# Optimization experiments

Measured on AMD Instinct MI355X. Metric: run time of the kernel, lower is better.

The kernel has to match this reference:

```python
import jax, jax.numpy as jnp
import numpy as np

DIM = 256          # dim_m == dim_d (required by hist @ W1)
HIST = 200         # history_num
B = 2048
U_TOT = 100000
V_TOT = 100000
EPS = 1e-12


def _max_norm_lookup(table, idx):
    # torch nn.Embedding(max_norm=1): rows are renormalized to L2 norm <= 1 at lookup.
    g = table[idx]
    n = jnp.linalg.norm(g, axis=-1, keepdims=True)
    return g * jnp.minimum(1.0, 1.0 / jnp.maximum(n, EPS))


def _l2norm(x):
    # F.normalize(x, 2, -1)
    return x / jnp.maximum(jnp.linalg.norm(x, axis=-1, keepdims=True), EPS)


def setup_inputs() -> dict:
    key = jax.random.key(0)
    ks = jax.random.split(key, 12)
    xav = float(np.sqrt(6.0 / (DIM + DIM)))
    xav_pb = float(np.sqrt(6.0 / (HIST + DIM)))
    return {
        "batch_u": jax.random.randint(ks[0], (B,), 0, U_TOT),
        "batch_v": jax.random.randint(ks[1], (B,), 0, V_TOT),
        "batch_history": jax.random.randint(ks[2], (B, HIST), 0, V_TOT),
        "batch_olc": jax.random.randint(ks[3], (B,), 0, 68),
        "batch_cluster_olc": jax.random.randint(ks[4], (B,), 0, 68),
        "user_emb": jax.random.normal(ks[5], (U_TOT, DIM), jnp.float32),
        "venue_emb": jax.random.normal(ks[6], (V_TOT, DIM), jnp.float32),
        "W1": jax.random.uniform(ks[7], (DIM, DIM), jnp.float32, -xav, xav),
        "W2": jax.random.uniform(ks[8], (DIM, DIM), jnp.float32, -xav, xav),
        "P": jax.random.normal(ks[9], (HIST, DIM), jnp.float32),
        "bias": jax.random.uniform(ks[10], (HIST, DIM), jnp.float32, -xav_pb, xav_pb),
        "a": jax.random.normal(ks[11], (1,), jnp.float32),
    }


def reference(batch_u, batch_v, batch_history, batch_olc, batch_cluster_olc,
              user_emb, venue_emb, W1, W2, P, bias, a):
    # batch_olc / batch_cluster_olc are read but unused in the original forward.
    u = _max_norm_lookup(user_emb, batch_u)            # [B, D]
    v = _max_norm_lookup(venue_emb, batch_v)           # [B, D]
    hist = _max_norm_lookup(venue_emb, batch_history)  # [B, H, D]

    # h = tanh(hist @ W1 + (P @ W2) + bias), broadcast over batch
    h = jnp.tanh(jnp.einsum('bhd,de->bhe', hist, W1) + (P @ W2)[None] + bias[None])
    alpha = jax.nn.softmax(h, axis=1)                  # softmax over history dim
    l = jnp.sum(alpha * hist, axis=1) + a              # [B, D], scalar a broadcast

    # TransE-style score with p_norm = 2
    s = _l2norm(u) + _l2norm(l) - _l2norm(v)
    return jnp.sqrt(jnp.sum(s * s, axis=-1))           # [B]
```

## Files before the change

kernel.cpp:

```cpp
#include <hip/hip_runtime.h>

#define DIM 256
#define HIST 200
#define MPAD 208
#define BATCH 2048
#define HSTRIDE 264
#define EPSF 1e-12f

typedef __bf16 bf16x8 __attribute__((ext_vector_type(8)));
typedef float f32x4 __attribute__((ext_vector_type(4)));

__device__ __forceinline__ unsigned short f2bf(float f) {
    union { float f; unsigned u; } v; v.f = f;
    unsigned r = (v.u + 0x7fffu + ((v.u >> 16) & 1u)) >> 16;
    return (unsigned short)r;
}
__device__ __forceinline__ float bf2f(unsigned short u) {
    union { unsigned u; float f; } v; v.u = ((unsigned)u) << 16;
    return v.f;
}

__global__ __launch_bounds__(256) void k_prep(
    const float* __restrict__ W1, const float* __restrict__ P,
    const float* __restrict__ W2, const float* __restrict__ bias,
    const float* __restrict__ venue,
    unsigned short* __restrict__ W1t2, float* __restrict__ Ct2,
    float* __restrict__ sInv, int nV) {
    const int bid = blockIdx.x, tid = threadIdx.x;
    if (bid < 16) {
#pragma unroll
        for (int it = 0; it < 16; ++it) {
            int idx = bid * 4096 + it * 256 + tid;
            int g = idx >> 11, rem = idx & 2047;
            int n = rem >> 3, j = rem & 7;
            W1t2[idx] = f2bf(W1[(g * 8 + j) * DIM + n]);
        }
    } else if (bid < 224) {
        const int h = bid - 16;
        __shared__ float Prow[DIM];
        const int e = tid;
        float acc = 0.f;
        if (h < HIST) {
            Prow[e] = P[h * DIM + e];
            __syncthreads();
            acc = bias[h * DIM + e];
#pragma unroll 8
            for (int d = 0; d < DIM; ++d) acc += Prow[d] * W2[d * DIM + e];
        }
        Ct2[((h >> 4) * 4 + ((h >> 2) & 3)) * 1024 + e * 4 + (h & 3)] = acc;
    } else {
        const int row = (bid - 224) * 4 + (tid >> 6);
        if (row >= nV) return;
        const int lane = tid & 63;
        const float4 g = *(const float4*)(venue + (size_t)row * DIM + lane * 4);
        float ss = g.x * g.x + g.y * g.y + g.z * g.z + g.w * g.w;
#pragma unroll
        for (int off = 32; off > 0; off >>= 1) ss += __shfl_xor(ss, off);
        if (lane == 0) sInv[row] = fminf(1.f, 1.f / fmaxf(sqrtf(ss), EPSF));
    }
}

__global__ __launch_bounds__(1024, 4) void k_main(
    const int* __restrict__ batch_u, const int* __restrict__ batch_v,
    const int* __restrict__ batch_history,
    const float* __restrict__ user_emb, const float* __restrict__ venue_emb,
    const float* __restrict__ Ct2, const unsigned short* __restrict__ W1t2,
    const float* __restrict__ sInv,
    const float* __restrict__ a_ptr, float* __restrict__ out) {

    __shared__ unsigned short histS[MPAD * HSTRIDE];
    __shared__ float scaleS[MPAD];
    __shared__ int idxS[MPAD];
    __shared__ float lArr[DIM];
    __shared__ float redS[4][4];
    __shared__ float invS[3];

    const int b = blockIdx.x;
    const int tid = threadIdx.x;
    const int wave = tid >> 6;
    const int lane = tid & 63;
    const int quad = lane >> 4;
    const int l16 = lane & 15;
    const int n = wave * 16 + l16;

    if (tid < MPAD) {
        int m = (tid < HIST) ? tid : 0;
        int ix = batch_history[b * HIST + m];
        idxS[tid] = ix;
        scaleS[tid] = sInv[ix];
    }
    __syncthreads();

    const int r0 = wave * 13;
    float4 buf[13];
#pragma unroll
    for (int j = 0; j < 13; ++j)
        buf[j] = *(const float4*)(venue_emb + (size_t)idxS[r0 + j] * DIM + lane * 4);
#pragma unroll
    for (int j = 0; j < 13; ++j) {
        float s = scaleS[r0 + j];
        ushort4 pk = { f2bf(buf[j].x * s), f2bf(buf[j].y * s),
                       f2bf(buf[j].z * s), f2bf(buf[j].w * s) };
        *(ushort4*)&histS[(r0 + j) * HSTRIDE + lane * 4] = pk;
    }

    f32x4 acc[13];
#pragma unroll
    for (int mt = 0; mt < 13; ++mt)
        acc[mt] = *(const f32x4*)(Ct2 + (mt * 4 + quad) * 1024 + n * 4);

    float ut = 0.f, vt = 0.f;
    if (tid < DIM) {
        ut = user_emb[(size_t)batch_u[b] * DIM + tid];
        vt = venue_emb[(size_t)batch_v[b] * DIM + tid];
    }
    __syncthreads();

#pragma unroll
    for (int k = 0; k < 8; ++k) {
        const bf16x8 Bf = *(const bf16x8*)(const void*)(W1t2 + (k * 4 + quad) * 2048 + n * 8);
#pragma unroll
        for (int mt = 0; mt < 13; ++mt) {
            const bf16x8 Af =
                *(const bf16x8*)(const void*)(&histS[(mt * 16 + l16) * HSTRIDE + k * 32 + quad * 8]);
            acc[mt] = __builtin_amdgcn_mfma_f32_16x16x32_bf16(Af, Bf, acc[mt], 0, 0, 0);
        }
    }

    const float a_val = a_ptr[0];
    float Ssum = 0.f, Lnum = 0.f;
#pragma unroll
    for (int mt = 0; mt < 13; ++mt)
#pragma unroll
        for (int r = 0; r < 4; ++r) {
            int m = mt * 16 + quad * 4 + r;
            if (m < HIST) {
                float x = acc[mt][r];
                float e2 = __expf(2.f * x);
                float th = 1.f - 2.f / (e2 + 1.f);
                float e = __expf(th);
                Ssum += e;
                Lnum += e * bf2f(histS[m * HSTRIDE + n]);
            }
        }
    Ssum += __shfl_xor(Ssum, 16); Ssum += __shfl_xor(Ssum, 32);
    Lnum += __shfl_xor(Lnum, 16); Lnum += __shfl_xor(Lnum, 32);
    if (quad == 0) lArr[n] = Lnum / Ssum + a_val;
    __syncthreads();

    const float lt = (tid < DIM) ? lArr[tid] : 0.f;
    float pu = ut * ut, pv = vt * vt, pl = lt * lt;
#pragma unroll
    for (int off = 32; off > 0; off >>= 1) {
        pu += __shfl_xor(pu, off);
        pv += __shfl_xor(pv, off);
        pl += __shfl_xor(pl, off);
    }
    if (lane == 0 && wave < 4) { redS[wave][0] = pu; redS[wave][1] = pv; redS[wave][2] = pl; }
    __syncthreads();
    if (tid == 0) {
        float su = 0.f, sv = 0.f, sl = 0.f;
        for (int w = 0; w < 4; ++w) { su += redS[w][0]; sv += redS[w][1]; sl += redS[w][2]; }
        invS[0] = 1.f / fmaxf(sqrtf(su), EPSF);
        invS[1] = 1.f / fmaxf(sqrtf(sv), EPSF);
        invS[2] = 1.f / fmaxf(sqrtf(sl), EPSF);
    }
    __syncthreads();
    float s = ut * invS[0] + lt * invS[2] - vt * invS[1];
    float s2 = s * s;
#pragma unroll
    for (int off = 32; off > 0; off >>= 1) s2 += __shfl_xor(s2, off);
    if (lane == 0 && wave < 4) redS[wave][3] = s2;
    __syncthreads();
    if (tid == 0) out[b] = sqrtf(redS[0][3] + redS[1][3] + redS[2][3] + redS[3][3]);
}

extern "C" void kernel_launch(void* const* d_in, const int* in_sizes, int n_in,
                              void* d_out, int out_size, void* d_ws, size_t ws_size,
                              hipStream_t stream) {
    const int* batch_u = (const int*)d_in[0];
    const int* batch_v = (const int*)d_in[1];
    const int* batch_history = (const int*)d_in[2];
    const float* user_emb = (const float*)d_in[5];
    const float* venue_emb = (const float*)d_in[6];
    const float* W1 = (const float*)d_in[7];
    const float* W2 = (const float*)d_in[8];
    const float* P = (const float*)d_in[9];
    const float* bias = (const float*)d_in[10];
    const float* a = (const float*)d_in[11];
    float* out = (float*)d_out;

    const int nV = in_sizes[6] / DIM;

    float* Ct2 = (float*)d_ws;
    unsigned short* W1t2 = (unsigned short*)((char*)d_ws + 212992);
    float* sInv = (float*)((char*)d_ws + 212992 + 131072);

    k_prep<<<224 + (nV + 3) / 4, 256, 0, stream>>>(W1, P, W2, bias, venue_emb,
                                                   W1t2, Ct2, sInv, nV);
    k_main<<<BATCH, 1024, 0, stream>>>(batch_u, batch_v, batch_history,
                                       user_emb, venue_emb, Ct2, W1t2, sInv, a, out);
}
```

Measured before the change: 413.1 us.

## Process history in two row chunks with 512-thread blocks and 2 N-tiles per wave

```diff
diff --git a/kernel.cpp b/kernel.cpp
--- a/kernel.cpp
+++ b/kernel.cpp
@@ -1,10 +1,12 @@
 #include <hip/hip_runtime.h>
+#include <hip/hip_bf16.h>
 
 #define DIM 256
 #define HIST 200
-#define MPAD 208
+#define MPAD2 224
+#define CHROWS 112
 #define BATCH 2048
-#define HSTRIDE 264
+#define HSTRIDE 280
 #define EPSF 1e-12f
 
 typedef __bf16 bf16x8 __attribute__((ext_vector_type(8)));
@@ -15,9 +17,15 @@
     unsigned r = (v.u + 0x7fffu + ((v.u >> 16) & 1u)) >> 16;
     return (unsigned short)r;
 }
-__device__ __forceinline__ float bf2f(unsigned short u) {
-    union { unsigned u; float f; } v; v.u = ((unsigned)u) << 16;
-    return v.f;
+__device__ __forceinline__ unsigned pkbf(float a, float b) {
+    __hip_bfloat162 t = __float22bfloat162_rn(float2{a, b});
+    union { __hip_bfloat162 h; unsigned u; } v; v.h = t; return v.u;
+}
+__device__ __forceinline__ float bf_lo(unsigned u) {
+    union { unsigned u; float f; } v; v.u = u << 16; return v.f;
+}
+__device__ __forceinline__ float bf_hi(unsigned u) {
+    union { unsigned u; float f; } v; v.u = u & 0xffff0000u; return v.f;
 }
 
 __global__ __launch_bounds__(256) void k_prep(
@@ -35,7 +43,7 @@
             int n = rem >> 3, j = rem & 7;
             W1t2[idx] = f2bf(W1[(g * 8 + j) * DIM + n]);
         }
-    } else if (bid < 224) {
+    } else if (bid < 240) {
         const int h = bid - 16;
         __shared__ float Prow[DIM];
         const int e = tid;
@@ -49,18 +57,18 @@
         }
         Ct2[((h >> 4) * 4 + ((h >> 2) & 3)) * 1024 + e * 4 + (h & 3)] = acc;
     } else {
-        const int row = (bid - 224) * 4 + (tid >> 6);
-        if (row >= nV) return;
         const int lane = tid & 63;
-        const float4 g = *(const float4*)(venue + (size_t)row * DIM + lane * 4);
-        float ss = g.x * g.x + g.y * g.y + g.z * g.z + g.w * g.w;
-#pragma unroll
-        for (int off = 32; off > 0; off >>= 1) ss += __shfl_xor(ss, off);
-        if (lane == 0) sInv[row] = fminf(1.f, 1.f / fmaxf(sqrtf(ss), EPSF));
-    }
-}
-
-__global__ __launch_bounds__(1024, 4) void k_main(
+        for (int row = (bid - 240) * 4 + (tid >> 6); row < nV; row += 1024) {
+            const float4 g = *(const float4*)(venue + (size_t)row * DIM + lane * 4);
+            float ss = g.x * g.x + g.y * g.y + g.z * g.z + g.w * g.w;
+#pragma unroll
+            for (int off = 32; off > 0; off >>= 1) ss += __shfl_xor(ss, off);
+            if (lane == 0) sInv[row] = fminf(1.f, 1.f / fmaxf(sqrtf(ss), EPSF));
+        }
+    }
+}
+
+__global__ __launch_bounds__(512, 4) void k_main(
     const int* __restrict__ batch_u, const int* __restrict__ batch_v,
     const int* __restrict__ batch_history,
     const float* __restrict__ user_emb, const float* __restrict__ venue_emb,
@@ -68,9 +76,9 @@
     const float* __restrict__ sInv,
     const float* __restrict__ a_ptr, float* __restrict__ out) {
 
-    __shared__ unsigned short histS[MPAD * HSTRIDE];
-    __shared__ float scaleS[MPAD];
-    __shared__ int idxS[MPAD];
+    __shared__ unsigned short histS[CHROWS * HSTRIDE];
+    __shared__ float scaleS[MPAD2];
+    __shared__ int idxS[MPAD2];
     __shared__ float lArr[DIM];
     __shared__ float redS[4][4];
     __shared__ float invS[3];
@@ -81,34 +89,14 @@
     const int lane = tid & 63;
     const int quad = lane >> 4;
     const int l16 = lane & 15;
-    const int n = wave * 16 + l16;
-
-    if (tid < MPAD) {
+    const int n0 = wave * 32 + l16 * 2;
+
+    if (tid < MPAD2) {
         int m = (tid < HIST) ? tid : 0;
         int ix = batch_history[b * HIST + m];
         idxS[tid] = ix;
-        scaleS[tid] = sInv[ix];
-    }
-    __syncthreads();
-
-    const int r0 = wave * 13;
-    float4 buf[13];
-#pragma unroll
-    for (int j = 0; j < 13; ++j)
-        buf[j] = *(const float4*)(venue_emb + (size_t)idxS[r0 + j] * DIM + lane * 4);
-#pragma unroll
-    for (int j = 0; j < 13; ++j) {
-        float s = scaleS[r0 + j];
-        ushort4 pk = { f2bf(buf[j].x * s), f2bf(buf[j].y * s),
-                       f2bf(buf[j].z * s), f2bf(buf[j].w * s) };
-        *(ushort4*)&histS[(r0 + j) * HSTRIDE + lane * 4] = pk;
-    }
-
-    f32x4 acc[13];
-#pragma unroll
-    for (int mt = 0; mt < 13; ++mt)
-        acc[mt] = *(const f32x4*)(Ct2 + (mt * 4 + quad) * 1024 + n * 4);
-
+        scaleS[tid] = (tid < HIST) ? sInv[ix] : 0.f;
+    }
     float ut = 0.f, vt = 0.f;
     if (tid < DIM) {
         ut = user_emb[(size_t)batch_u[b] * DIM + tid];
@@ -116,36 +104,75 @@
     }
     __syncthreads();
 
-#pragma unroll
-    for (int k = 0; k < 8; ++k) {
-        const bf16x8 Bf = *(const bf16x8*)(const void*)(W1t2 + (k * 4 + quad) * 2048 + n * 8);
-#pragma unroll
-        for (int mt = 0; mt < 13; ++mt) {
-            const bf16x8 Af =
-                *(const bf16x8*)(const void*)(&histS[(mt * 16 + l16) * HSTRIDE + k * 32 + quad * 8]);
-            acc[mt] = __builtin_amdgcn_mfma_f32_16x16x32_bf16(Af, Bf, acc[mt], 0, 0, 0);
-        }
-    }
-
     const float a_val = a_ptr[0];
-    float Ssum = 0.f, Lnum = 0.f;
-#pragma unroll
-    for (int mt = 0; mt < 13; ++mt)
-#pragma unroll
-        for (int r = 0; r < 4; ++r) {
-            int m = mt * 16 + quad * 4 + r;
-            if (m < HIST) {
-                float x = acc[mt][r];
-                float e2 = __expf(2.f * x);
-                float th = 1.f - 2.f / (e2 + 1.f);
-                float e = __expf(th);
-                Ssum += e;
-                Lnum += e * bf2f(histS[m * HSTRIDE + n]);
+    float Ssum[2] = {0.f, 0.f}, Lnum[2] = {0.f, 0.f};
+
+    for (int chunk = 0; chunk < 2; ++chunk) {
+        const int base = chunk * CHROWS;
+        const int r0 = wave * 14;
+#pragma unroll
+        for (int half = 0; half < 2; ++half) {
+            float4 buf[7];
+#pragma unroll
+            for (int j = 0; j < 7; ++j)
+                buf[j] = *(const float4*)(venue_emb +
+                         (size_t)idxS[base + r0 + half * 7 + j] * DIM + lane * 4);
+#pragma unroll
+            for (int j = 0; j < 7; ++j) {
+                int lr = r0 + half * 7 + j;
+                float s = scaleS[base + lr];
+                uint2 pk = { pkbf(buf[j].x * s, buf[j].y * s),
+                             pkbf(buf[j].z * s, buf[j].w * s) };
+                *(uint2*)&histS[lr * HSTRIDE + lane * 4] = pk;
             }
         }
-    Ssum += __shfl_xor(Ssum, 16); Ssum += __shfl_xor(Ssum, 32);
-    Lnum += __shfl_xor(Lnum, 16); Lnum += __shfl_xor(Lnum, 32);
-    if (quad == 0) lArr[n] = Lnum / Ssum + a_val;
+        f32x4 acc[7][2];
+#pragma unroll
+        for (int t = 0; t < 7; ++t)
+#pragma unroll
+            for (int i = 0; i < 2; ++i)
+                acc[t][i] = *(const f32x4*)(Ct2 + ((chunk * 7 + t) * 4 + quad) * 1024 + (n0 + i) * 4);
+        __syncthreads();
+
+#pragma unroll
+        for (int k = 0; k < 8; ++k) {
+            bf16x8 Bf0 = *(const bf16x8*)(const void*)(W1t2 + (k * 4 + quad) * 2048 + n0 * 8);
+            bf16x8 Bf1 = *(const bf16x8*)(const void*)(W1t2 + (k * 4 + quad) * 2048 + (n0 + 1) * 8);
+#pragma unroll
+            for (int t = 0; t < 7; ++t) {
+                const bf16x8 Af =
+                    *(const bf16x8*)(const void*)(&histS[(t * 16 + l16) * HSTRIDE + k * 32 + quad * 8]);
+                acc[t][0] = __builtin_amdgcn_mfma_f32_16x16x32_bf16(Af, Bf0, acc[t][0], 0, 0, 0);
+                acc[t][1] = __builtin_amdgcn_mfma_f32_16x16x32_bf16(Af, Bf1, acc[t][1], 0, 0, 0);
+            }
+        }
+
+#pragma unroll
+        for (int t = 0; t < 7; ++t)
+#pragma unroll
+            for (int r = 0; r < 4; ++r) {
+                int lm = t * 16 + quad * 4 + r;
+                if (base + lm < HIST) {
+                    unsigned hv = *(const unsigned*)&histS[lm * HSTRIDE + n0];
+                    float x0 = acc[t][0][r], x1 = acc[t][1][r];
+                    float th0 = 1.f - 2.f * __builtin_amdgcn_rcpf(__expf(2.f * x0) + 1.f);
+                    float th1 = 1.f - 2.f * __builtin_amdgcn_rcpf(__expf(2.f * x1) + 1.f);
+                    float e0 = __expf(th0), e1 = __expf(th1);
+                    Ssum[0] += e0; Lnum[0] += e0 * bf_lo(hv);
+                    Ssum[1] += e1; Lnum[1] += e1 * bf_hi(hv);
+                }
+            }
+        __syncthreads();
+    }
+
+#pragma unroll
+    for (int i = 0; i < 2; ++i) {
+        Ssum[i] += __shfl_xor(Ssum[i], 16); Ssum[i] += __shfl_xor(Ssum[i], 32);
+        Lnum[i] += __shfl_xor(Lnum[i], 16); Lnum[i] += __shfl_xor(Lnum[i], 32);
+    }
+    if (quad == 0)
+        *(float2*)&lArr[n0] = float2{ Lnum[0] * __builtin_amdgcn_rcpf(Ssum[0]) + a_val,
+                                      Lnum[1] * __builtin_amdgcn_rcpf(Ssum[1]) + a_val };
     __syncthreads();
 
     const float lt = (tid < DIM) ? lArr[tid] : 0.f;
@@ -193,11 +220,10 @@
     const int nV = in_sizes[6] / DIM;
 
     float* Ct2 = (float*)d_ws;
-    unsigned short* W1t2 = (unsigned short*)((char*)d_ws + 212992);
-    float* sInv = (float*)((char*)d_ws + 212992 + 131072);
-
-    k_prep<<<224 + (nV + 3) / 4, 256, 0, stream>>>(W1, P, W2, bias, venue_emb,
-                                                   W1t2, Ct2, sInv, nV);
-    k_main<<<BATCH, 1024, 0, stream>>>(batch_u, batch_v, batch_history,
-                                       user_emb, venue_emb, Ct2, W1t2, sInv, a, out);
-}
+    unsigned short* W1t2 = (unsigned short*)((char*)d_ws + 229376);
+    float* sInv = (float*)((char*)d_ws + 229376 + 131072);
+
+    k_prep<<<496, 256, 0, stream>>>(W1, P, W2, bias, venue_emb, W1t2, Ct2, sInv, nV);
+    k_main<<<BATCH, 512, 0, stream>>>(batch_u, batch_v, batch_history,
+                                      user_emb, venue_emb, Ct2, W1t2, sInv, a, out);
+}
```

Result: slower. 480.3 us (+16.3%).
